# Kernel tuning notes

Measured on AMD Instinct MI355X. Metric: run time of the kernel, lower is better.

## Reference

```python
import jax, jax.numpy as jnp
import numpy as np

B, L, NT = 4, 512, 20
H, DK, DM = 6, 10, 60  # heads, d_k, d_model (=embedding_dim+1)
ED = 59


def setup_inputs() -> dict:
    key = jax.random.key(0)
    ks = jax.random.split(key, 12)
    # event_seqs[..., 0] = event times (increasing), event_seqs[..., 1] = event type id stored as float
    times = jnp.cumsum(jax.random.uniform(ks[0], (B, L + 1)), axis=1)
    types = jax.random.randint(ks[1], (B, L + 1), 0, NT).astype(jnp.float32)
    event_seqs = jnp.stack([times, types], axis=-1)  # [B, L+1, 2]
    # causal (subsequent) mask, no padding -> lower-triangular [B, L, L]
    src_mask = jnp.broadcast_to(jnp.tril(jnp.ones((L, L), dtype=bool)), (B, L, L))
    w = lambda k, s: jax.random.normal(k, s, dtype=jnp.float32) * 0.1
    return dict(
        event_seqs=event_seqs, src_mask=src_mask,
        embed_w=w(ks[2], (ED, NT)),
        q_w=w(ks[3], (DM, DM)), q_b=jnp.zeros((DM,), jnp.float32),
        k_w=w(ks[4], (DM, DM)), k_b=jnp.zeros((DM,), jnp.float32),
        v_w=w(ks[5], (DM, DM)), v_b=jnp.zeros((DM,), jnp.float32),
        alpha_w=w(ks[6], (DK, DK * H // 2)), alpha_b=jnp.zeros((DK,), jnp.float32),
        gamma_w=w(ks[7], (DK, DK * H // 2)), gamma_b=jnp.zeros((DK,), jnp.float32),
        mu_w=w(ks[8], (DK, DM)), mu_b=jnp.zeros((DK,), jnp.float32),
    )


def reference(event_seqs, src_mask, embed_w, q_w, q_b, k_w, k_b, v_w, v_b,
              alpha_w, alpha_b, gamma_w, gamma_b, mu_w, mu_b):
    b = event_seqs.shape[0]
    # temporal feature: dt between consecutive events (ts padded with leading 0)
    ts = jnp.pad(event_seqs[:, :, 0], ((0, 0), (1, 0)))  # [B, T+1]
    dt = ts[:, 1:] - ts[:, :-1]                           # [B, T]
    temp_feat = dt[:, :-1, None]                          # [B, L, 1]
    types = event_seqs[:, :-1, 1].astype(jnp.int32)       # [B, L]
    type_feat = jax.nn.one_hot(types, NT, dtype=jnp.float32) @ embed_w.T  # [B, L, ED]
    feat = jnp.concatenate([temp_feat, type_feat], axis=-1)  # [B, L, DM]

    def heads(x, w, bias):
        return (x @ w.T + bias).reshape(b, L, H, DK).transpose(0, 2, 1, 3)  # [B,H,L,DK]

    q = heads(feat, q_w, q_b)
    k = heads(feat, k_w, k_b)
    v = heads(feat, v_w, v_b)

    mask4 = src_mask[:, None, :, :]  # [B,1,L,L]
    scores = jnp.einsum('bhid,bhjd->bhij', q, k) / np.sqrt(DK).astype(np.float32)
    scores = jnp.where(mask4, scores, -1e9)
    p_attn = jax.nn.softmax(scores, axis=-1)
    p_attn = jnp.where(mask4, p_attn, 0.0)               # [B,H,L,L]
    v_mu_pre = jnp.einsum('bhij,bhjd->bhid', p_attn, v)  # [B,H,L,DK]

    # per-pair attn * value, split heads in half (faithful to torch view semantics)
    prod = p_attn[..., None] * v[:, :, None, :, :]       # [B,H,L,L,DK]
    hh = H // 2
    x_alpha = prod[:, :hh].reshape(b, L, L, hh * DK)     # raw C-order reshape == torch .view
    x_gamma = prod[:, hh:].reshape(b, L, L, hh * DK)

    v_alpha = jax.nn.softplus(x_alpha @ alpha_w.T + alpha_b)          # Softplus(beta=1)
    v_gamma = jax.nn.softplus(10.0 * (x_gamma @ gamma_w.T + gamma_b)) / 10.0  # Softplus(beta=10)
    pair_mask = src_mask[..., None]                      # [B,L,L,1]
    v_alpha = jnp.where(pair_mask, v_alpha, 0.0)
    v_gamma = jnp.where(pair_mask, v_gamma, 0.0)

    v_mu = jax.nn.sigmoid(v_mu_pre.transpose(0, 2, 1, 3).reshape(b, L, DM) @ mu_w.T + mu_b)  # [B,L,DK]
    return (v_mu, v_alpha, v_gamma)
```

## Files before the change

kernel.cpp:

```cpp
#include <hip/hip_runtime.h>
#include <hip/hip_bf16.h>

#define BB 4
#define LL 512
#define NTYPES 20
#define HH 6
#define DKK 10
#define DMM 60
#define PROW 516
#define NWROW 516

__device__ __forceinline__ float softplus_fast(float x) {
    return fmaxf(x, 0.0f) + __logf(1.0f + __expf(-fabsf(x)));
}

__global__ void ishp_qkv(const float* __restrict__ ev,
                         const float* __restrict__ embed_w,
                         const float* __restrict__ qw, const float* __restrict__ qb,
                         const float* __restrict__ kw, const float* __restrict__ kb,
                         const float* __restrict__ vw, const float* __restrict__ vb,
                         const float* __restrict__ aw, const float* __restrict__ gw,
                         float* __restrict__ q, float* __restrict__ kT, float* __restrict__ vT,
                         float* __restrict__ Wbuf)
{
    int pos = blockIdx.x;
    int b = pos >> 9, l = pos & 511;
    __shared__ float feat[DMM];
    __shared__ float sv[DMM];
    int t = threadIdx.x;
    if (t == 0) {
        float t1 = ev[(b * (LL + 1) + l) * 2 + 0];
        float t0 = (l > 0) ? ev[(b * (LL + 1) + l - 1) * 2 + 0] : 0.0f;
        feat[0] = t1 - t0;
    } else if (t < DMM) {
        int type = (int)ev[(b * (LL + 1) + l) * 2 + 1];
        feat[t] = embed_w[(t - 1) * NTYPES + type];
    }
    __syncthreads();
    if (t < 3 * DMM) {
        int which = t / DMM;
        int m = t - which * DMM;
        const float* w  = which == 0 ? qw : which == 1 ? kw : vw;
        const float* bs = which == 0 ? qb : which == 1 ? kb : vb;
        float s = bs[m];
        #pragma unroll
        for (int c = 0; c < DMM; ++c) s += feat[c] * w[m * DMM + c];
        int h = m / DKK, d = m - h * DKK;
        if (which == 0)      q [((b * HH + h) * LL + l) * DKK + d] = s;
        else if (which == 1) kT[((b * HH + h) * DKK + d) * LL + l] = s;
        else {
            vT[((b * HH + h) * DKK + d) * LL + l] = s;
            sv[m] = s;
        }
    }
    __syncthreads();
    if (t < 180) {
        int kk = t % 10;
        int u = t / 10;
        int h  = u % 3;
        int cc = (u / 3) % 3;
        int mat = u / 9;
        const float* w = mat ? gw : aw;
        float s = 0.0f;
        #pragma unroll
        for (int d = 0; d < DKK; ++d) s += w[kk * 30 + cc * 10 + d] * sv[(h + 3 * mat) * DKK + d];
        int slot = (l % 3) * 172 + l / 3;
        Wbuf[((size_t)((((mat * 3 + cc) * 4 + b) * 3 + h) * 10 + kk)) * NWROW + slot] = s;
    }
}

__global__ __launch_bounds__(256) void ishp_attn(const float* __restrict__ q,
                                                 const float* __restrict__ kT,
                                                 const float* __restrict__ vT,
                                                 __hip_bfloat16* __restrict__ pbuf,
                                                 float* __restrict__ vmupre)
{
    __shared__ float sK[DKK * LL];
    __shared__ float sV[DKK * LL];
    int bh = blockIdx.x >> 4;
    int rg = blockIdx.x & 15;
    int tid = threadIdx.x;
    int lane = tid & 63;
    int wv = tid >> 6;

    const float4* kT4 = reinterpret_cast<const float4*>(kT + (size_t)bh * DKK * LL);
    const float4* vT4 = reinterpret_cast<const float4*>(vT + (size_t)bh * DKK * LL);
    float4* sK4 = reinterpret_cast<float4*>(sK);
    float4* sV4 = reinterpret_cast<float4*>(sV);
    #pragma unroll
    for (int u = 0; u < 5; ++u) {
        int idx = u * 256 + tid;
        sK4[idx] = kT4[idx];
        sV4[idx] = vT4[idx];
    }
    __syncthreads();

    const float scale = 0.31622776601683794f;

    for (int t = 0; t < 8; ++t) {
        int i = rg + 16 * (wv + 4 * t);
        float qr[DKK];
        #pragma unroll
        for (int d = 0; d < DKK; ++d) qr[d] = q[((size_t)bh * LL + i) * DKK + d];
        int nchunk = (i >> 6) + 1;

        float e[8];
        float S = 0.0f;
        #pragma unroll
        for (int c = 0; c < 8; ++c) {
            e[c] = 0.0f;
            if (c < nchunk) {
                int j = c * 64 + lane;
                float dot = 0.0f;
                #pragma unroll
                for (int d = 0; d < DKK; ++d) dot += qr[d] * sK[d * LL + j];
                if (j <= i) e[c] = __expf(dot * scale);
                S += e[c];
            }
        }
        #pragma unroll
        for (int off = 32; off >= 1; off >>= 1) S += __shfl_xor(S, off, 64);
        float inv = 1.0f / S;

        __hip_bfloat16* prow = pbuf + (size_t)(bh * LL + i) * PROW;
        #pragma unroll
        for (int c = 0; c < 8; ++c) {
            if (c < nchunk) {
                int j = c * 64 + lane;
                int slot = (j % 3) * 172 + j / 3;
                if (j <= i) prow[slot] = __float2bfloat16(e[c] * inv);
            }
        }

        float acc[DKK];
        #pragma unroll
        for (int d = 0; d < DKK; ++d) acc[d] = 0.0f;
        #pragma unroll
        for (int c = 0; c < 8; ++c) {
            if (c < nchunk) {
                int j = c * 64 + lane;
                #pragma unroll
                for (int d = 0; d < DKK; ++d) acc[d] += e[c] * sV[d * LL + j];
            }
        }
        #pragma unroll
        for (int d = 0; d < DKK; ++d) {
            float a = acc[d];
            #pragma unroll
            for (int off = 32; off >= 1; off >>= 1) a += __shfl_xor(a, off, 64);
            acc[d] = a;
        }
        if (lane == 0) {
            #pragma unroll
            for (int d = 0; d < DKK; ++d)
                vmupre[((size_t)bh * LL + i) * DKK + d] = acc[d] * inv;
        }
    }
}

__global__ __launch_bounds__(256) void ishp_ag(const __hip_bfloat16* __restrict__ pbuf,
                                               const float* __restrict__ Wbuf,
                                               const float* __restrict__ ab,
                                               const float* __restrict__ gb,
                                               const float* __restrict__ vmupre,
                                               const float* __restrict__ muw,
                                               const float* __restrict__ mub,
                                               float* __restrict__ out_mu,
                                               float* __restrict__ outA,
                                               float* __restrict__ outG)
{
    __shared__ float sA[2560];
    __shared__ float sG[2560];
    int tid = threadIdx.x;
    int pos = blockIdx.x * 256 + tid;
    int b  = pos >> 18;
    int i2 = (pos >> 9) & 511;
    int j2 = pos & 511;

    float ra[DKK], rg[DKK];
    if (j2 > i2) {
        #pragma unroll
        for (int kk = 0; kk < DKK; ++kk) { ra[kk] = 0.0f; rg[kk] = 0.0f; }
    } else {
        #pragma unroll
        for (int kk = 0; kk < DKK; ++kk) { ra[kk] = ab[kk]; rg[kk] = gb[kk]; }
        #pragma unroll
        for (int cc = 0; cc < 3; ++cc) {
            int u = 3 * j2 + cc;
            int sel = u >> 9;
            int j = u & 511;
            int hi = 3 * i2 + sel;
            int h = hi >> 9;
            int i = hi & 511;
            int jq = j / 3;
            int r = j - 3 * jq;
            int slot = r * 172 + jq;
            float pa = 0.0f, pg = 0.0f;
            if (j <= i) {
                pa = __bfloat162float(pbuf[(size_t)((b * HH + h) * LL + i) * PROW + slot]);
                pg = __bfloat162float(pbuf[(size_t)((b * HH + h + 3) * LL + i) * PROW + slot]);
            }
            const float* Wa = Wbuf + ((size_t)(((0 + cc) * 4 + b) * 3 + h) * 10) * NWROW + slot;
            const float* Wg = Wbuf + ((size_t)(((3 + cc) * 4 + b) * 3 + h) * 10) * NWROW + slot;
            #pragma unroll
            for (int kk = 0; kk < DKK; ++kk) {
                ra[kk] += pa * Wa[kk * NWROW];
                rg[kk] += pg * Wg[kk * NWROW];
            }
        }
        #pragma unroll
        for (int kk = 0; kk < DKK; ++kk) {
            ra[kk] = softplus_fast(ra[kk]);
            rg[kk] = softplus_fast(10.0f * rg[kk]) * 0.1f;
        }
    }
    #pragma unroll
    for (int kk = 0; kk < DKK; ++kk) { sA[tid * 10 + kk] = ra[kk]; sG[tid * 10 + kk] = rg[kk]; }
    __syncthreads();

    size_t base = (size_t)blockIdx.x * 2560;
    #pragma unroll
    for (int it = 0; it < 3; ++it) {
        int idx = it * 1024 + tid * 4;
        if (idx < 2560) {
            *reinterpret_cast<float4*>(outA + base + idx) = *reinterpret_cast<const float4*>(&sA[idx]);
            *reinterpret_cast<float4*>(outG + base + idx) = *reinterpret_cast<const float4*>(&sG[idx]);
        }
    }

    if (blockIdx.x < 8) {
        int mpos = blockIdx.x * 256 + tid;
        int mb = mpos >> 9, ml = mpos & 511;
        float y[DKK];
        #pragma unroll
        for (int kk = 0; kk < DKK; ++kk) y[kk] = mub[kk];
        for (int c = 0; c < DMM; ++c) {
            int h = c / DKK, d = c - h * DKK;
            float xc = vmupre[((mb * HH + h) * LL + ml) * DKK + d];
            #pragma unroll
            for (int kk = 0; kk < DKK; ++kk) y[kk] += xc * muw[kk * DMM + c];
        }
        #pragma unroll
        for (int kk = 0; kk < DKK; ++kk)
            out_mu[(size_t)mpos * DKK + kk] = 1.0f / (1.0f + __expf(-y[kk]));
    }
}

extern "C" void kernel_launch(void* const* d_in, const int* in_sizes, int n_in,
                              void* d_out, int out_size, void* d_ws, size_t ws_size,
                              hipStream_t stream) {
    const void *ev = 0, *emb = 0, *muw = 0;
    const void *w3[3] = {0, 0, 0}, *b3[3] = {0, 0, 0};
    const void *w300[2] = {0, 0};
    const void *b10[3] = {0, 0, 0};
    int n3 = 0, nb3 = 0, n300 = 0, n10 = 0;
    for (int i = 0; i < n_in; ++i) {
        int s = in_sizes[i];
        if      (s == 4104) ev  = d_in[i];
        else if (s == 1180) emb = d_in[i];
        else if (s == 600)  muw = d_in[i];
        else if (s == 3600) { if (n3  < 3) w3[n3++]   = d_in[i]; }
        else if (s == 60)   { if (nb3 < 3) b3[nb3++]  = d_in[i]; }
        else if (s == 300)  { if (n300< 2) w300[n300++]=d_in[i]; }
        else if (s == 10)   { if (n10 < 3) b10[n10++] = d_in[i]; }
    }

    float* ws = (float*)d_ws;
    float* q = ws;
    float* kT = q + 122880;
    float* vT = kT + 122880;
    float* vmupre = vT + 122880;
    float* Wbuf = vmupre + 122880;
    __hip_bfloat16* pbuf = (__hip_bfloat16*)(Wbuf + 371520);

    float* out = (float*)d_out;
    float* out_mu = out;
    float* out_a  = out + 20480;
    float* out_g  = out + 20480 + 10485760;

    ishp_qkv<<<BB * LL, 192, 0, stream>>>((const float*)ev, (const float*)emb,
        (const float*)w3[0], (const float*)b3[0],
        (const float*)w3[1], (const float*)b3[1],
        (const float*)w3[2], (const float*)b3[2],
        (const float*)w300[0], (const float*)w300[1],
        q, kT, vT, Wbuf);
    ishp_attn<<<BB * HH * 16, 256, 0, stream>>>(q, kT, vT, pbuf, vmupre);
    ishp_ag<<<(BB * LL * LL) / 256, 256, 0, stream>>>(pbuf, Wbuf,
        (const float*)b10[0], (const float*)b10[1], vmupre,
        (const float*)muw, (const float*)b10[2], out_mu, out_a, out_g);
}
```

Measured before the change: 64.96 us.

## Spread attention rows across more blocks with balanced causal row pairing

```diff
diff --git a/kernel.cpp b/kernel.cpp
--- a/kernel.cpp
+++ b/kernel.cpp
@@ -69,93 +69,84 @@
     }
 }
 
+__device__ __forceinline__ void attn_row(int bh, int i, int lane,
+        const float* __restrict__ q, const float* __restrict__ kT_,
+        const float* __restrict__ vT_,
+        __hip_bfloat16* __restrict__ pbuf, float* __restrict__ vmupre)
+{
+    const float scale = 0.31622776601683794f;
+    float qr[DKK];
+    #pragma unroll
+    for (int d = 0; d < DKK; ++d) qr[d] = q[((size_t)bh * LL + i) * DKK + d];
+    int nchunk = (i >> 6) + 1;
+
+    float e[8];
+    float S = 0.0f;
+    #pragma unroll
+    for (int c = 0; c < 8; ++c) {
+        e[c] = 0.0f;
+        if (c < nchunk) {
+            int j = c * 64 + lane;
+            float dot = 0.0f;
+            #pragma unroll
+            for (int d = 0; d < DKK; ++d) dot += qr[d] * kT_[d * LL + j];
+            if (j <= i) e[c] = __expf(dot * scale);
+            S += e[c];
+        }
+    }
+    #pragma unroll
+    for (int off = 32; off >= 1; off >>= 1) S += __shfl_xor(S, off, 64);
+    float inv = 1.0f / S;
+
+    __hip_bfloat16* prow = pbuf + (size_t)(bh * LL + i) * PROW;
+    #pragma unroll
+    for (int c = 0; c < 8; ++c) {
+        if (c < nchunk) {
+            int j = c * 64 + lane;
+            int slot = (j % 3) * 172 + j / 3;
+            if (j <= i) prow[slot] = __float2bfloat16(e[c] * inv);
+        }
+    }
+
+    float acc[DKK];
+    #pragma unroll
+    for (int d = 0; d < DKK; ++d) acc[d] = 0.0f;
+    #pragma unroll
+    for (int c = 0; c < 8; ++c) {
+        if (c < nchunk) {
+            int j = c * 64 + lane;
+            #pragma unroll
+            for (int d = 0; d < DKK; ++d) acc[d] += e[c] * vT_[d * LL + j];
+        }
+    }
+    #pragma unroll
+    for (int d = 0; d < DKK; ++d) {
+        float a = acc[d];
+        #pragma unroll
+        for (int off = 32; off >= 1; off >>= 1) a += __shfl_xor(a, off, 64);
+        acc[d] = a;
+    }
+    if (lane == 0) {
+        #pragma unroll
+        for (int d = 0; d < DKK; ++d)
+            vmupre[((size_t)bh * LL + i) * DKK + d] = acc[d] * inv;
+    }
+}
+
 __global__ __launch_bounds__(256) void ishp_attn(const float* __restrict__ q,
                                                  const float* __restrict__ kT,
                                                  const float* __restrict__ vT,
                                                  __hip_bfloat16* __restrict__ pbuf,
                                                  float* __restrict__ vmupre)
 {
-    __shared__ float sK[DKK * LL];
-    __shared__ float sV[DKK * LL];
-    int bh = blockIdx.x >> 4;
-    int rg = blockIdx.x & 15;
-    int tid = threadIdx.x;
-    int lane = tid & 63;
-    int wv = tid >> 6;
-
-    const float4* kT4 = reinterpret_cast<const float4*>(kT + (size_t)bh * DKK * LL);
-    const float4* vT4 = reinterpret_cast<const float4*>(vT + (size_t)bh * DKK * LL);
-    float4* sK4 = reinterpret_cast<float4*>(sK);
-    float4* sV4 = reinterpret_cast<float4*>(sV);
-    #pragma unroll
-    for (int u = 0; u < 5; ++u) {
-        int idx = u * 256 + tid;
-        sK4[idx] = kT4[idx];
-        sV4[idx] = vT4[idx];
-    }
-    __syncthreads();
-
-    const float scale = 0.31622776601683794f;
-
-    for (int t = 0; t < 8; ++t) {
-        int i = rg + 16 * (wv + 4 * t);
-        float qr[DKK];
-        #pragma unroll
-        for (int d = 0; d < DKK; ++d) qr[d] = q[((size_t)bh * LL + i) * DKK + d];
-        int nchunk = (i >> 6) + 1;
-
-        float e[8];
-        float S = 0.0f;
-        #pragma unroll
-        for (int c = 0; c < 8; ++c) {
-            e[c] = 0.0f;
-            if (c < nchunk) {
-                int j = c * 64 + lane;
-                float dot = 0.0f;
-                #pragma unroll
-                for (int d = 0; d < DKK; ++d) dot += qr[d] * sK[d * LL + j];
-                if (j <= i) e[c] = __expf(dot * scale);
-                S += e[c];
-            }
-        }
-        #pragma unroll
-        for (int off = 32; off >= 1; off >>= 1) S += __shfl_xor(S, off, 64);
-        float inv = 1.0f / S;
-
-        __hip_bfloat16* prow = pbuf + (size_t)(bh * LL + i) * PROW;
-        #pragma unroll
-        for (int c = 0; c < 8; ++c) {
-            if (c < nchunk) {
-                int j = c * 64 + lane;
-                int slot = (j % 3) * 172 + j / 3;
-                if (j <= i) prow[slot] = __float2bfloat16(e[c] * inv);
-            }
-        }
-
-        float acc[DKK];
-        #pragma unroll
-        for (int d = 0; d < DKK; ++d) acc[d] = 0.0f;
-        #pragma unroll
-        for (int c = 0; c < 8; ++c) {
-            if (c < nchunk) {
-                int j = c * 64 + lane;
-                #pragma unroll
-                for (int d = 0; d < DKK; ++d) acc[d] += e[c] * sV[d * LL + j];
-            }
-        }
-        #pragma unroll
-        for (int d = 0; d < DKK; ++d) {
-            float a = acc[d];
-            #pragma unroll
-            for (int off = 32; off >= 1; off >>= 1) a += __shfl_xor(a, off, 64);
-            acc[d] = a;
-        }
-        if (lane == 0) {
-            #pragma unroll
-            for (int d = 0; d < DKK; ++d)
-                vmupre[((size_t)bh * LL + i) * DKK + d] = acc[d] * inv;
-        }
-    }
+    int lane = threadIdx.x & 63;
+    int gw = blockIdx.x * 4 + (threadIdx.x >> 6);
+    int bh = gw >> 8;
+    int p = gw & 255;
+    const float* kT_ = kT + (size_t)bh * DKK * LL;
+    const float* vT_ = vT + (size_t)bh * DKK * LL;
+    attn_row(bh, 511 - p, lane, q, kT_, vT_, pbuf, vmupre);
+    attn_row(bh, p, lane, q, kT_, vT_, pbuf, vmupre);
 }
 
 __global__ __launch_bounds__(256) void ishp_ag(const __hip_bfloat16* __restrict__ pbuf,
@@ -284,7 +275,7 @@
         (const float*)w3[2], (const float*)b3[2],
         (const float*)w300[0], (const float*)w300[1],
         q, kT, vT, Wbuf);
-    ishp_attn<<<BB * HH * 16, 256, 0, stream>>>(q, kT, vT, pbuf, vmupre);
+    ishp_attn<<<(BB * HH * LL) / 8, 256, 0, stream>>>(q, kT, vT, pbuf, vmupre);
     ishp_ag<<<(BB * LL * LL) / 256, 256, 0, stream>>>(pbuf, Wbuf,
         (const float*)b10[0], (const float*)b10[1], vmupre,
         (const float*)muw, (const float*)b10[2], out_mu, out_a, out_g);
```

Result: faster. 59.57 us (-8.3%).

## Balance causal attention rows per wave and store K/V row-major with in-LDS transpose

Applied to the files above, without the earlier changes.

```diff
diff --git a/kernel.cpp b/kernel.cpp
--- a/kernel.cpp
+++ b/kernel.cpp
@@ -20,7 +20,7 @@
                          const float* __restrict__ kw, const float* __restrict__ kb,
                          const float* __restrict__ vw, const float* __restrict__ vb,
                          const float* __restrict__ aw, const float* __restrict__ gw,
-                         float* __restrict__ q, float* __restrict__ kT, float* __restrict__ vT,
+                         float* __restrict__ q, float* __restrict__ kR, float* __restrict__ vR,
                          float* __restrict__ Wbuf)
 {
     int pos = blockIdx.x;
@@ -46,10 +46,11 @@
         #pragma unroll
         for (int c = 0; c < DMM; ++c) s += feat[c] * w[m * DMM + c];
         int h = m / DKK, d = m - h * DKK;
-        if (which == 0)      q [((b * HH + h) * LL + l) * DKK + d] = s;
-        else if (which == 1) kT[((b * HH + h) * DKK + d) * LL + l] = s;
+        size_t off = ((size_t)(b * HH + h) * LL + l) * DKK + d;
+        if (which == 0)      q [off] = s;
+        else if (which == 1) kR[off] = s;
         else {
-            vT[((b * HH + h) * DKK + d) * LL + l] = s;
+            vR[off] = s;
             sv[m] = s;
         }
     }
@@ -70,90 +71,98 @@
 }
 
 __global__ __launch_bounds__(256) void ishp_attn(const float* __restrict__ q,
-                                                 const float* __restrict__ kT,
-                                                 const float* __restrict__ vT,
+                                                 const float* __restrict__ kR,
+                                                 const float* __restrict__ vR,
                                                  __hip_bfloat16* __restrict__ pbuf,
                                                  float* __restrict__ vmupre)
 {
     __shared__ float sK[DKK * LL];
     __shared__ float sV[DKK * LL];
-    int bh = blockIdx.x >> 4;
-    int rg = blockIdx.x & 15;
+    int bh = blockIdx.x >> 5;
+    int rg = blockIdx.x & 31;
     int tid = threadIdx.x;
     int lane = tid & 63;
     int wv = tid >> 6;
 
-    const float4* kT4 = reinterpret_cast<const float4*>(kT + (size_t)bh * DKK * LL);
-    const float4* vT4 = reinterpret_cast<const float4*>(vT + (size_t)bh * DKK * LL);
-    float4* sK4 = reinterpret_cast<float4*>(sK);
-    float4* sV4 = reinterpret_cast<float4*>(sV);
+    const float2* k2 = reinterpret_cast<const float2*>(kR + (size_t)bh * DKK * LL);
+    const float2* v2 = reinterpret_cast<const float2*>(vR + (size_t)bh * DKK * LL);
     #pragma unroll
-    for (int u = 0; u < 5; ++u) {
+    for (int u = 0; u < 10; ++u) {
         int idx = u * 256 + tid;
-        sK4[idx] = kT4[idx];
-        sV4[idx] = vT4[idx];
+        int l = idx / 5, dp = idx % 5;
+        float2 kv = k2[idx];
+        sK[(2 * dp) * LL + l] = kv.x;
+        sK[(2 * dp + 1) * LL + l] = kv.y;
+        float2 vv = v2[idx];
+        sV[(2 * dp) * LL + l] = vv.x;
+        sV[(2 * dp + 1) * LL + l] = vv.y;
     }
     __syncthreads();
 
     const float scale = 0.31622776601683794f;
 
-    for (int t = 0; t < 8; ++t) {
-        int i = rg + 16 * (wv + 4 * t);
-        float qr[DKK];
-        #pragma unroll
-        for (int d = 0; d < DKK; ++d) qr[d] = q[((size_t)bh * LL + i) * DKK + d];
-        int nchunk = (i >> 6) + 1;
-
-        float e[8];
-        float S = 0.0f;
-        #pragma unroll
-        for (int c = 0; c < 8; ++c) {
-            e[c] = 0.0f;
-            if (c < nchunk) {
-                int j = c * 64 + lane;
-                float dot = 0.0f;
+    #pragma unroll
+    for (int sidx = 0; sidx < 2; ++sidx) {
+        int P = rg * 8 + wv + 4 * sidx;
+        #pragma unroll
+        for (int half = 0; half < 2; ++half) {
+            int i = half == 0 ? (511 - P) : P;
+            float qr[DKK];
+            #pragma unroll
+            for (int d = 0; d < DKK; ++d) qr[d] = q[((size_t)bh * LL + i) * DKK + d];
+            int nchunk = (i >> 6) + 1;
+
+            float e[8];
+            float S = 0.0f;
+            #pragma unroll
+            for (int c = 0; c < 8; ++c) {
+                e[c] = 0.0f;
+                if (c < nchunk) {
+                    int j = c * 64 + lane;
+                    float dot = 0.0f;
+                    #pragma unroll
+                    for (int d = 0; d < DKK; ++d) dot += qr[d] * sK[d * LL + j];
+                    if (j <= i) e[c] = __expf(dot * scale);
+                    S += e[c];
+                }
+            }
+            #pragma unroll
+            for (int off = 32; off >= 1; off >>= 1) S += __shfl_xor(S, off, 64);
+            float inv = 1.0f / S;
+
+            __hip_bfloat16* prow = pbuf + (size_t)(bh * LL + i) * PROW;
+            #pragma unroll
+            for (int c = 0; c < 8; ++c) {
+                if (c < nchunk) {
+                    int j = c * 64 + lane;
+                    int slot = (j % 3) * 172 + j / 3;
+                    if (j <= i) prow[slot] = __float2bfloat16(e[c] * inv);
+                }
+            }
+
+            float acc[DKK];
+            #pragma unroll
+            for (int d = 0; d < DKK; ++d) acc[d] = 0.0f;
+            #pragma unroll
+            for (int c = 0; c < 8; ++c) {
+                if (c < nchunk) {
+                    int j = c * 64 + lane;
+                    #pragma unroll
+                    for (int d = 0; d < DKK; ++d) acc[d] += e[c] * sV[d * LL + j];
+                }
+            }
+            #pragma unroll
+            for (int d = 0; d < DKK; ++d) {
+                float a = acc[d];
                 #pragma unroll
-                for (int d = 0; d < DKK; ++d) dot += qr[d] * sK[d * LL + j];
-                if (j <= i) e[c] = __expf(dot * scale);
-                S += e[c];
-            }
-        }
-        #pragma unroll
-        for (int off = 32; off >= 1; off >>= 1) S += __shfl_xor(S, off, 64);
-        float inv = 1.0f / S;
-
-        __hip_bfloat16* prow = pbuf + (size_t)(bh * LL + i) * PROW;
-        #pragma unroll
-        for (int c = 0; c < 8; ++c) {
-            if (c < nchunk) {
-                int j = c * 64 + lane;
-                int slot = (j % 3) * 172 + j / 3;
-                if (j <= i) prow[slot] = __float2bfloat16(e[c] * inv);
-            }
-        }
-
-        float acc[DKK];
-        #pragma unroll
-        for (int d = 0; d < DKK; ++d) acc[d] = 0.0f;
-        #pragma unroll
-        for (int c = 0; c < 8; ++c) {
-            if (c < nchunk) {
-                int j = c * 64 + lane;
+                for (int off = 32; off >= 1; off >>= 1) a += __shfl_xor(a, off, 64);
+                acc[d] = a;
+            }
+            if (lane == 0) {
                 #pragma unroll
-                for (int d = 0; d < DKK; ++d) acc[d] += e[c] * sV[d * LL + j];
-            }
-        }
-        #pragma unroll
-        for (int d = 0; d < DKK; ++d) {
-            float a = acc[d];
-            #pragma unroll
-            for (int off = 32; off >= 1; off >>= 1) a += __shfl_xor(a, off, 64);
-            acc[d] = a;
-        }
-        if (lane == 0) {
-            #pragma unroll
-            for (int d = 0; d < DKK; ++d)
-                vmupre[((size_t)bh * LL + i) * DKK + d] = acc[d] * inv;
+                for (int d = 0; d < DKK; ++d)
+                    vmupre[((size_t)bh * LL + i) * DKK + d] = acc[d] * inv;
+            }
         }
     }
 }
@@ -267,9 +276,9 @@
 
     float* ws = (float*)d_ws;
     float* q = ws;
-    float* kT = q + 122880;
-    float* vT = kT + 122880;
-    float* vmupre = vT + 122880;
+    float* kR = q + 122880;
+    float* vR = kR + 122880;
+    float* vmupre = vR + 122880;
     float* Wbuf = vmupre + 122880;
     __hip_bfloat16* pbuf = (__hip_bfloat16*)(Wbuf + 371520);
 
@@ -283,8 +292,8 @@
         (const float*)w3[1], (const float*)b3[1],
         (const float*)w3[2], (const float*)b3[2],
         (const float*)w300[0], (const float*)w300[1],
-        q, kT, vT, Wbuf);
-    ishp_attn<<<BB * HH * 16, 256, 0, stream>>>(q, kT, vT, pbuf, vmupre);
+        q, kR, vR, Wbuf);
+    ishp_attn<<<BB * HH * 32, 256, 0, stream>>>(q, kR, vR, pbuf, vmupre);
     ishp_ag<<<(BB * LL * LL) / 256, 256, 0, stream>>>(pbuf, Wbuf,
         (const float*)b10[0], (const float*)b10[1], vmupre,
         (const float*)muw, (const float*)b10[2], out_mu, out_a, out_g);
```

Result: faster. 57.78 us (-11.0%).
